# Performance work log

Hardware: AMD Instinct MI355X
Metric: run time of the kernel (lower is better)

## Reference

```python
import jax, jax.numpy as jnp
import numpy as np

N, D, K = 131072, 768, 2000


def setup_inputs() -> dict:
    key = jax.random.key(0)
    kx, kc = jax.random.split(key)
    x = jax.random.normal(kx, (N, D), dtype=jnp.float32)
    centroids = jax.random.normal(kc, (D, K), dtype=jnp.float32)  # stored as [D, K] like the torch module
    return {"x": x, "centroids": centroids}


def reference(x, centroids):
    # dist[n,k] = ||x_n||^2 - 2 x_n . c_k + ||c_k||^2  (matmul trick)
    x_norm = jnp.sum(x * x, axis=1, keepdims=True)              # [N, 1]
    c_norm = jnp.sum(centroids * centroids, axis=0, keepdims=True)  # [1, K]
    dist = x_norm - 2.0 * jnp.matmul(x, centroids) + c_norm     # [N, K]
    return jnp.argmin(dist, axis=-1)                            # [N] int
```

## Files before the change

### kernel.cpp

```cpp
#include <hip/hip_runtime.h>
#include <hip/hip_bf16.h>

#define N_ROWS 131072
#define DIM    768
#define K_C    2000
#define K_PAD  2048
#define TAU    0.2f
#define LISTCAP 8192

typedef _Float16 f16;
typedef _Float16 f16x4 __attribute__((ext_vector_type(4)));
typedef _Float16 f16x8 __attribute__((ext_vector_type(8)));
typedef float    f32x4 __attribute__((ext_vector_type(4)));

#define OFF_CN   6291456
#define OFF_XN   6299648
#define OFF_PMIN 6823936
#define OFF_PSEC 15212544
#define OFF_PIDX 23601152
#define OFF_CNT  31989760
#define OFF_LIST 31990016
#define OFF_CN64 32022784
#define OFF_XH   32039168

static __device__ __forceinline__ void gload16(const void* g, void* l) {
  __builtin_amdgcn_global_load_lds(
      (const __attribute__((address_space(1))) unsigned int*)g,
      (__attribute__((address_space(3))) unsigned int*)l, 16, 0, 0);
}

__global__ __launch_bounds__(256) void prep_cn(const float* __restrict__ cent,
                                               float* __restrict__ cn,
                                               double* __restrict__ cn64) {
#pragma clang fp contract(off)
  __shared__ float pf[8][32];
  __shared__ double pd[8][32];
  int t = threadIdx.x;
  int kk = t & 31;
  int k = blockIdx.x * 32 + kk;
  int p = t >> 5;
  float s = 0.0f;
  double s64 = 0.0;
  for (int d = p * 96; d < p * 96 + 96; ++d) {
    float c = (k < K_C) ? cent[d * K_C + k] : 0.0f;
    float sq = c * c;
    s = s + sq;
    s64 += (double)c * (double)c;
  }
  pf[p][kk] = s;
  pd[p][kk] = s64;
  __syncthreads();
  if (p == 0) {
    float ss = 0.0f;
    double ss64 = 0.0;
#pragma unroll
    for (int q = 0; q < 8; ++q) {
      ss = ss + pf[q][kk];
      ss64 += pd[q][kk];
    }
    cn[k] = (k < K_C) ? ss : INFINITY;
    cn64[k] = (k < K_C) ? ss64 : (double)INFINITY;
  }
}

__global__ __launch_bounds__(256) void prep_ct(const float* __restrict__ cent,
                                               f16* __restrict__ cTh) {
  __shared__ float ld[64][65];
  int k0 = blockIdx.x * 64;
  int d0 = blockIdx.y * 64;
  int tid = threadIdx.x;
#pragma unroll
  for (int it = 0; it < 16; ++it) {
    int idx = it * 256 + tid;
    int dd = idx >> 6, kk = idx & 63;
    int k = k0 + kk;
    ld[dd][kk] = (k < K_C) ? cent[(size_t)(d0 + dd) * K_C + k] : 0.0f;
  }
  __syncthreads();
#pragma unroll
  for (int it = 0; it < 16; ++it) {
    int idx = it * 256 + tid;
    int kk = idx >> 6, dd = idx & 63;
    cTh[(size_t)(k0 + kk) * DIM + d0 + dd] = (f16)ld[dd][kk];
  }
}

__global__ __launch_bounds__(256) void xnorm_prepx(const float* __restrict__ x,
                                                   float* __restrict__ xn,
                                                   f16* __restrict__ xh) {
#pragma clang fp contract(off)
  __shared__ __align__(16) float buf[16 * DIM];
  int row0 = blockIdx.x * 16;
  int tid = threadIdx.x;
  const f32x4* src = (const f32x4*)(x + (size_t)row0 * DIM);
  f32x4* dst = (f32x4*)buf;
#pragma unroll
  for (int c = 0; c < 12; ++c) {
    f32x4 v = src[c * 256 + tid];
    dst[c * 256 + tid] = v;
    f16x4 hv;
#pragma unroll
    for (int j = 0; j < 4; ++j) hv[j] = (f16)v[j];
    *(f16x4*)(xh + (size_t)row0 * DIM + (size_t)(c * 256 + tid) * 4) = hv;
  }
  __syncthreads();
  int w = tid >> 6, lane = tid & 63;
  int b = lane >> 3, j = lane & 7;
#pragma unroll
  for (int rr = 0; rr < 4; ++rr) {
    int r = w * 4 + rr;
    const float* a = buf + r * DIM + 96 * b + j;
    float v0 = a[0];
    float acc = v0 * v0;
#pragma unroll
    for (int t = 1; t < 12; ++t) {
      float q = a[8 * t];
      float s = q * q;
      acc = acc + s;
    }
    float v = acc;
    { float o = __shfl_xor(v, 1);  v = v + o; }
    { float o = __shfl_xor(v, 2);  v = v + o; }
    { float o = __shfl_xor(v, 4);  v = v + o; }
    { float o = __shfl_xor(v, 8);  v = v + o; }
    { float o = __shfl_xor(v, 16); v = v + o; }
    { float o = __shfl_xor(v, 32); v = v + o; }
    if (lane == 0) xn[row0 + r] = v;
  }
}

#define STAGE3(bufo)                                                           \
  do {                                                                         \
    gload16(pA0, ldsb + (bufo) + c0 * 1024);                                   \
    gload16(pA1, ldsb + (bufo) + c1 * 1024);                                   \
    gload16(pB0, ldsb + 24576 + (bufo) + c0 * 1024);                           \
    gload16(pB1, ldsb + 24576 + (bufo) + c1 * 1024);                           \
    pA0 += 64; pA1 += 64; pB0 += 64; pB1 += 64;                                \
  } while (0)

__global__ __launch_bounds__(256, 3) void kmeans_main(
    const f16* __restrict__ xh, const f16* __restrict__ cTh,
    const float* __restrict__ cn, const float* __restrict__ xn,
    float* __restrict__ pmin, float* __restrict__ psec,
    int* __restrict__ pidx) {
  __shared__ __align__(16) f16 lds[24576];
  char* ldsb = (char*)lds;

  int d0 = blockIdx.x;
  int g  = (d0 & 7) * 2048 + (d0 >> 3);
  int pb = g & 15;
  int rb = g >> 4;

  int tid  = threadIdx.x;
  int w    = tid >> 6;
  int lane = tid & 63;
  int wrow = (w >> 1) * 64;
  int wcol = (w & 1) * 64;

  int rsel = lane & 15;
  int ksel = lane >> 4;
  int rs = (ksel ^ ((rsel >> 1) & 3)) << 4;

  int c0 = w * 2, c1 = w * 2 + 1;
  int grn = (lane & 3) ^ ((lane >> 3) & 3);
  const char* pA0 = (const char*)xh +
      ((size_t)(rb * 128 + c0 * 16 + (lane >> 2)) * DIM + grn * 8) * 2;
  const char* pA1 = (const char*)xh +
      ((size_t)(rb * 128 + c1 * 16 + (lane >> 2)) * DIM + grn * 8) * 2;
  const char* pB0 = (const char*)cTh +
      ((size_t)(pb * 128 + c0 * 16 + (lane >> 2)) * DIM + grn * 8) * 2;
  const char* pB1 = (const char*)cTh +
      ((size_t)(pb * 128 + c1 * 16 + (lane >> 2)) * DIM + grn * 8) * 2;

  f32x4 acc[4][4] = {};

  STAGE3(0);
  STAGE3(8192);

  int cb = 0;
  int sb = 16384;
#pragma unroll 3
  for (int kt = 0; kt < 24; ++kt) {
    if (kt < 23) {
      asm volatile("s_waitcnt vmcnt(4)" ::: "memory");
    } else {
      asm volatile("s_waitcnt vmcnt(0)" ::: "memory");
    }
    __builtin_amdgcn_sched_barrier(0);
    __builtin_amdgcn_s_barrier();
    __builtin_amdgcn_sched_barrier(0);

    if (kt < 22) STAGE3(sb);

    f16x8 ah[4], bh[4];
    int abase = cb + (wrow + rsel) * 64 + rs;
    int bbase = cb + 24576 + (wcol + rsel) * 64 + rs;
#pragma unroll
    for (int m = 0; m < 4; ++m) ah[m] = *(const f16x8*)(ldsb + abase + m * 1024);
#pragma unroll
    for (int n = 0; n < 4; ++n) bh[n] = *(const f16x8*)(ldsb + bbase + n * 1024);

    __builtin_amdgcn_s_setprio(1);
#pragma unroll
    for (int m = 0; m < 4; ++m)
#pragma unroll
      for (int n = 0; n < 4; ++n)
        acc[m][n] = __builtin_amdgcn_mfma_f32_16x16x32_f16(ah[m], bh[n],
                                                           acc[m][n], 0, 0, 0);
    __builtin_amdgcn_s_setprio(0);

    cb = (cb == 16384) ? 0 : cb + 8192;
    sb = (sb == 16384) ? 0 : sb + 8192;
  }

  __syncthreads();
  float* lv = (float*)lds;
  float* lsv = (float*)lds + 256;
  int*   li = (int*)((float*)lds + 512);

  int colbase = pb * 128 + wcol + rsel;
  float cnv[4];
#pragma unroll
  for (int n = 0; n < 4; ++n) cnv[n] = cn[colbase + n * 16];
  int g4 = ksel * 4;

#pragma unroll
  for (int m = 0; m < 4; ++m) {
#pragma unroll
    for (int j = 0; j < 4; ++j) {
      int trow = wrow + m * 16 + g4 + j;
      float xv = xn[rb * 128 + trow];
      float v1 = 0.0f, v2 = INFINITY;
      int i1 = 0;
#pragma unroll
      for (int n = 0; n < 4; ++n) {
        float dd = (xv - 2.0f * acc[m][n][j]) + cnv[n];
        int ci = colbase + n * 16;
        if (n == 0) { v1 = dd; i1 = ci; }
        else if (dd < v1) { v2 = v1; v1 = dd; i1 = ci; }
        else { v2 = fminf(v2, dd); }
      }
#pragma unroll
      for (int off = 1; off < 16; off <<= 1) {
        float ov1 = __shfl_xor(v1, off);
        float ov2 = __shfl_xor(v2, off);
        int oi1 = __shfl_xor(i1, off);
        if (ov1 < v1 || (ov1 == v1 && oi1 < i1)) {
          v2 = fminf(v1, ov2); v1 = ov1; i1 = oi1;
        } else {
          v2 = fminf(v2, ov1);
        }
      }
      if ((lane & 15) == 0) {
        lv[(w & 1) * 128 + trow] = v1;
        lsv[(w & 1) * 128 + trow] = v2;
        li[(w & 1) * 128 + trow] = i1;
      }
    }
  }
  __syncthreads();
  if (tid < 128) {
    float a1 = lv[tid], a2 = lsv[tid];
    int aj = li[tid];
    float b1 = lv[128 + tid], b2 = lsv[128 + tid];
    int bj = li[128 + tid];
    float v1, v2; int i1;
    if (b1 < a1 || (b1 == a1 && bj < aj)) { v1 = b1; i1 = bj; v2 = fminf(b2, a1); }
    else { v1 = a1; i1 = aj; v2 = fminf(a2, b1); }
    size_t o = (size_t)pb * N_ROWS + rb * 128 + tid;
    pmin[o] = v1;
    psec[o] = v2;
    pidx[o] = i1;
  }
}

__global__ void merge_detect(const float* __restrict__ pmin,
                             const float* __restrict__ psec,
                             const int* __restrict__ pidx, int* __restrict__ out,
                             int* __restrict__ list, int* __restrict__ counter) {
  int n = blockIdx.x * 256 + threadIdx.x;
  float v1 = INFINITY, v2 = INFINITY;
  int i1 = 0x7fffffff;
  for (int p = 0; p < 16; ++p) {
    float a1 = pmin[(size_t)p * N_ROWS + n];
    float a2 = psec[(size_t)p * N_ROWS + n];
    int aj = pidx[(size_t)p * N_ROWS + n];
    if (a1 < v1 || (a1 == v1 && aj < i1)) {
      v2 = fminf(v1, a2); v1 = a1; i1 = aj;
    } else {
      v2 = fminf(v2, a1);
    }
  }
  out[n] = i1;
  if (v2 - v1 < TAU) {
    int idx = atomicAdd(counter, 1);
    if (idx < LISTCAP) list[idx] = n;
  }
}

#define ACCS(R) \
  double a##R##0 = 0, a##R##1 = 0, a##R##2 = 0, a##R##3 = 0, \
         a##R##4 = 0, a##R##5 = 0, a##R##6 = 0, a##R##7 = 0
#define FMAS(R, XV) \
  a##R##0 = fma(XV, c0, a##R##0); a##R##1 = fma(XV, c1, a##R##1); \
  a##R##2 = fma(XV, c2, a##R##2); a##R##3 = fma(XV, c3, a##R##3); \
  a##R##4 = fma(XV, c4, a##R##4); a##R##5 = fma(XV, c5, a##R##5); \
  a##R##6 = fma(XV, c6, a##R##6); a##R##7 = fma(XV, c7, a##R##7)
#define EVAL(R)                                                         \
  {                                                                     \
    double dots[8] = {a##R##0, a##R##1, a##R##2, a##R##3,               \
                      a##R##4, a##R##5, a##R##6, a##R##7};              \
    double bv = (double)INFINITY;                                       \
    int bi = 0x7fffffff;                                                \
    _Pragma("unroll") for (int j = 0; j < 8; ++j) {                     \
      int k = tid + j * 256;                                            \
      if (k < K_C) {                                                    \
        double dd = (xnorms[R] - 2.0 * dots[j]) + cn64[k];              \
        if (dd < bv) { bv = dd; bi = k; }                               \
      }                                                                 \
    }                                                                   \
    rv[tid] = bv; ri[tid] = bi;                                         \
    __syncthreads();                                                    \
    for (int s = 128; s > 0; s >>= 1) {                                 \
      if (tid < s) {                                                    \
        double ov = rv[tid + s];                                        \
        int oi = ri[tid + s];                                           \
        if (ov < rv[tid] || (ov == rv[tid] && oi < ri[tid])) {          \
          rv[tid] = ov; ri[tid] = oi;                                   \
        }                                                               \
      }                                                                 \
      __syncthreads();                                                  \
    }                                                                   \
    if (tid == 0 && (R) < nrows) out[list[b0 + (R)]] = ri[0];           \
    __syncthreads();                                                    \
  }

__global__ __launch_bounds__(256) void exact_recheck64(
    const float* __restrict__ x, const float* __restrict__ cent,
    const double* __restrict__ cn64, const int* __restrict__ list,
    const int* __restrict__ counter, int* __restrict__ out) {
  __shared__ __align__(16) float xrow[2][DIM];
  __shared__ double rv[256];
  __shared__ int ri[256];
  __shared__ double xnorms[2];
  int cnt = counter[0];
  if (cnt > LISTCAP) cnt = LISTCAP;
  int b0 = blockIdx.x * 2;
  if (b0 >= cnt) return;
  int nrows = cnt - b0;
  if (nrows > 2) nrows = 2;
  int tid = threadIdx.x;
  for (int r = 0; r < 2; ++r) {
    int n = list[b0 + (r < nrows ? r : 0)];
    double part = 0.0;
    for (int d = tid; d < DIM; d += 256) {
      float v = x[(size_t)n * DIM + d];
      xrow[r][d] = v;
      part += (double)v * (double)v;
    }
    rv[tid] = part;
    __syncthreads();
    for (int s = 128; s > 0; s >>= 1) {
      if (tid < s) rv[tid] += rv[tid + s];
      __syncthreads();
    }
    if (tid == 0) xnorms[r] = rv[0];
    __syncthreads();
  }

  int k7 = tid + 1792;
  int k7c = (k7 < K_C) ? k7 : (K_C - 1);
  ACCS(0); ACCS(1);
#pragma unroll 2
  for (int d = 0; d < DIM; ++d) {
    const float* cp = cent + (size_t)d * K_C + tid;
    double c0 = cp[0], c1 = cp[256], c2 = cp[512], c3 = cp[768];
    double c4 = cp[1024], c5 = cp[1280], c6 = cp[1536];
    double c7 = cp[k7c - tid];
    double x0 = xrow[0][d], x1 = xrow[1][d];
    FMAS(0, x0); FMAS(1, x1);
  }
  EVAL(0) EVAL(1)
}

extern "C" void kernel_launch(void* const* d_in, const int* in_sizes, int n_in,
                              void* d_out, int out_size, void* d_ws, size_t ws_size,
                              hipStream_t stream) {
  const float* x = (const float*)d_in[0];
  const float* cent = (const float*)d_in[1];
  char* ws = (char*)d_ws;
  f16* cTh = (f16*)ws;
  float* cn = (float*)(ws + OFF_CN);
  float* xn = (float*)(ws + OFF_XN);
  float* pmin = (float*)(ws + OFF_PMIN);
  float* psec = (float*)(ws + OFF_PSEC);
  int* pidx = (int*)(ws + OFF_PIDX);
  int* counter = (int*)(ws + OFF_CNT);
  int* list = (int*)(ws + OFF_LIST);
  double* cn64 = (double*)(ws + OFF_CN64);
  f16* xh = (f16*)(ws + OFF_XH);

  hipMemsetAsync(counter, 0, 4, stream);
  prep_cn<<<64, 256, 0, stream>>>(cent, cn, cn64);
  prep_ct<<<dim3(32, 12), 256, 0, stream>>>(cent, cTh);
  xnorm_prepx<<<N_ROWS / 16, 256, 0, stream>>>(x, xn, xh);
  kmeans_main<<<16384, 256, 0, stream>>>(xh, cTh, cn, xn, pmin, psec, pidx);
  merge_detect<<<N_ROWS / 256, 256, 0, stream>>>(pmin, psec, pidx, (int*)d_out,
                                                 list, counter);
  exact_recheck64<<<LISTCAP / 2, 256, 0, stream>>>(x, cent, cn64, list, counter,
                                                   (int*)d_out);
}
```

Baseline: 1.036 ms.

## Load X operand directly to registers from a pre-tiled layout, bypassing LDS

The x-to-f16 prep kernel now writes X in a panel/k-tile permuted layout that matches the MFMA fragment order. The main GEMM loop loads A fragments straight from global memory into registers, so only the centroid tile is staged in LDS. Shared memory per block is halved and the launch bound is raised to four blocks per CU to increase occupancy. In exchange, A-load latency is no longer covered by the LDS double buffer, and the two waves sharing the same rows both fetch them redundantly from cache. The epilogue also reuses the smaller LDS buffer, which is a correctness risk if it needed the old size.

Measured after the change: 1.180 ms. 13.9% more time.

```diff
diff --git a/kernel.cpp b/kernel.cpp
--- a/kernel.cpp
+++ b/kernel.cpp
@@ -87,7 +87,7 @@
 
 __global__ __launch_bounds__(256) void xnorm_prepx(const float* __restrict__ x,
                                                    float* __restrict__ xn,
-                                                   f16* __restrict__ xh) {
+                                                   f16* __restrict__ xhT) {
 #pragma clang fp contract(off)
   __shared__ __align__(16) float buf[16 * DIM];
   int row0 = blockIdx.x * 16;
@@ -101,7 +101,14 @@
     f16x4 hv;
 #pragma unroll
     for (int j = 0; j < 4; ++j) hv[j] = (f16)v[j];
-    *(f16x4*)(xh + (size_t)row0 * DIM + (size_t)(c * 256 + tid) * 4) = hv;
+    int flat4 = (c * 256 + tid) * 4;
+    int r = flat4 / DIM;
+    int k = flat4 - r * DIM;
+    int n = row0 + r;
+    int panel = n >> 7, pr = n & 127;
+    int kt = k >> 5, g = (k >> 3) & 3, sub = k & 7;
+    size_t idx = (size_t)panel * 98304 + kt * 4096 + pr * 32 + g * 8 + sub;
+    *(f16x4*)(xhT + idx) = hv;
   }
   __syncthreads();
   int w = tid >> 6, lane = tid & 63;
@@ -131,19 +138,17 @@
 
 #define STAGE3(bufo)                                                           \
   do {                                                                         \
-    gload16(pA0, ldsb + (bufo) + c0 * 1024);                                   \
-    gload16(pA1, ldsb + (bufo) + c1 * 1024);                                   \
-    gload16(pB0, ldsb + 24576 + (bufo) + c0 * 1024);                           \
-    gload16(pB1, ldsb + 24576 + (bufo) + c1 * 1024);                           \
-    pA0 += 64; pA1 += 64; pB0 += 64; pB1 += 64;                                \
+    gload16(pB0, ldsb + (bufo) + c0 * 1024);                                   \
+    gload16(pB1, ldsb + (bufo) + c1 * 1024);                                   \
+    pB0 += 64; pB1 += 64;                                                      \
   } while (0)
 
-__global__ __launch_bounds__(256, 3) void kmeans_main(
-    const f16* __restrict__ xh, const f16* __restrict__ cTh,
+__global__ __launch_bounds__(256, 4) void kmeans_main(
+    const f16* __restrict__ xhT, const f16* __restrict__ cTh,
     const float* __restrict__ cn, const float* __restrict__ xn,
     float* __restrict__ pmin, float* __restrict__ psec,
     int* __restrict__ pidx) {
-  __shared__ __align__(16) f16 lds[24576];
+  __shared__ __align__(16) f16 lds[12288];
   char* ldsb = (char*)lds;
 
   int d0 = blockIdx.x;
@@ -163,14 +168,13 @@
 
   int c0 = w * 2, c1 = w * 2 + 1;
   int grn = (lane & 3) ^ ((lane >> 3) & 3);
-  const char* pA0 = (const char*)xh +
-      ((size_t)(rb * 128 + c0 * 16 + (lane >> 2)) * DIM + grn * 8) * 2;
-  const char* pA1 = (const char*)xh +
-      ((size_t)(rb * 128 + c1 * 16 + (lane >> 2)) * DIM + grn * 8) * 2;
   const char* pB0 = (const char*)cTh +
       ((size_t)(pb * 128 + c0 * 16 + (lane >> 2)) * DIM + grn * 8) * 2;
   const char* pB1 = (const char*)cTh +
       ((size_t)(pb * 128 + c1 * 16 + (lane >> 2)) * DIM + grn * 8) * 2;
+
+  const char* aB = (const char*)xhT + (size_t)rb * 196608 +
+                   (wrow + rsel) * 64 + ksel * 16;
 
   f32x4 acc[4][4] = {};
 
@@ -182,7 +186,7 @@
 #pragma unroll 3
   for (int kt = 0; kt < 24; ++kt) {
     if (kt < 23) {
-      asm volatile("s_waitcnt vmcnt(4)" ::: "memory");
+      asm volatile("s_waitcnt vmcnt(2)" ::: "memory");
     } else {
       asm volatile("s_waitcnt vmcnt(0)" ::: "memory");
     }
@@ -190,13 +194,16 @@
     __builtin_amdgcn_s_barrier();
     __builtin_amdgcn_sched_barrier(0);
 
+    f16x8 ah[4];
+#pragma unroll
+    for (int m = 0; m < 4; ++m)
+      ah[m] = *(const f16x8*)(aB + m * 1024);
+    aB += 8192;
+
     if (kt < 22) STAGE3(sb);
 
-    f16x8 ah[4], bh[4];
-    int abase = cb + (wrow + rsel) * 64 + rs;
-    int bbase = cb + 24576 + (wcol + rsel) * 64 + rs;
-#pragma unroll
-    for (int m = 0; m < 4; ++m) ah[m] = *(const f16x8*)(ldsb + abase + m * 1024);
+    f16x8 bh[4];
+    int bbase = cb + (wcol + rsel) * 64 + rs;
 #pragma unroll
     for (int n = 0; n < 4; ++n) bh[n] = *(const f16x8*)(ldsb + bbase + n * 1024);
 
@@ -398,13 +405,13 @@
   int* counter = (int*)(ws + OFF_CNT);
   int* list = (int*)(ws + OFF_LIST);
   double* cn64 = (double*)(ws + OFF_CN64);
-  f16* xh = (f16*)(ws + OFF_XH);
+  f16* xhT = (f16*)(ws + OFF_XH);
 
   hipMemsetAsync(counter, 0, 4, stream);
   prep_cn<<<64, 256, 0, stream>>>(cent, cn, cn64);
   prep_ct<<<dim3(32, 12), 256, 0, stream>>>(cent, cTh);
-  xnorm_prepx<<<N_ROWS / 16, 256, 0, stream>>>(x, xn, xh);
-  kmeans_main<<<16384, 256, 0, stream>>>(xh, cTh, cn, xn, pmin, psec, pidx);
+  xnorm_prepx<<<N_ROWS / 16, 256, 0, stream>>>(x, xn, xhT);
+  kmeans_main<<<16384, 256, 0, stream>>>(xhT, cTh, cn, xn, pmin, psec, pidx);
   merge_detect<<<N_ROWS / 256, 256, 0, stream>>>(pmin, psec, pidx, (int*)d_out,
                                                  list, counter);
   exact_recheck64<<<LISTCAP / 2, 256, 0, stream>>>(x, cent, cn64, list, counter,
```
